# Optimization experiments

Hardware: AMD Instinct MI355X
Metric: run time of the kernel (lower is better)

## Reference

```python
import jax, jax.numpy as jnp
import numpy as np

# Quantization constants (match init_kwargs)
A_SCALE = 0.05   # activation scale
W_SCALE = 0.01   # weight scale
A_QN, A_QP = -128, 127  # int8 activation clamp range
STRIDE = (2, 2)
PADDING = ((1, 1), (1, 1))
DILATION = (1, 1)


def setup_inputs() -> dict:
    key = jax.random.key(0)
    kx, kw = jax.random.split(key)
    # Input activations [N, C_in, H, W]
    x = jax.random.normal(kx, (32, 256, 56, 56), dtype=jnp.float32)
    # Int4 weights in [-8, 7], stored as int-valued float32 (unpacked form of weight_packed)
    w = jax.random.randint(kw, (256, 256, 3, 3), -8, 8).astype(jnp.float32)
    return {"x": x, "w": w}


def reference(x, w):
    # Activation int8 quantization: round-half-to-even (matches torch.round), clamp to [a_qn, a_qp]
    x_q = jnp.clip(jnp.round(x / A_SCALE), A_QN, A_QP)
    # Int4xInt8 GEMM over unfolded patches == conv on quantized integer values.
    # Values are small ints so fp32 accumulation is exact (|acc| <= 2304*127*8 < 2^24).
    acc = jax.lax.conv_general_dilated(
        x_q, w,
        window_strides=STRIDE,
        padding=PADDING,
        rhs_dilation=DILATION,
        dimension_numbers=("NCHW", "OIHW", "NCHW"),
    )  # [N, C_out, H_out, W_out] = [32, 256, 28, 28]
    # Dequantize: acc_int32 * (a_scale * w_scale); bias=False; out_dtype=float32
    y = acc * (A_SCALE * W_SCALE)
    return y.astype(jnp.float32)
```

## Files before the change

kernel.cpp:

```cpp
#include <hip/hip_runtime.h>
#include <stdint.h>

typedef int v4i __attribute__((ext_vector_type(4)));

#define N_IMG 32
#define C_IN 256
#define H_IN 56
#define W_IN 56
#define C_OUT 256
#define H_OUT 28
#define W_OUT 28
#define H_PAD 58
#define W_PAD 58
#define SP_TOT (N_IMG*H_OUT*W_OUT)

#define XPAD_BYTES ((size_t)N_IMG*H_PAD*W_PAD*C_IN)


__device__ __forceinline__ void glds16(const int8_t* g, int8_t* l) {
    __builtin_amdgcn_global_load_lds(
        (const __attribute__((address_space(1))) void*)g,
        (__attribute__((address_space(3))) void*)l, 16, 0, 0);
}

__global__ __launch_bounds__(256, 4) void quant_kernel(const float* __restrict__ x,
                                                       int8_t* __restrict__ xpad) {
    __shared__ uint32_t ldsu[W_IN * 65];
    const int hp = blockIdx.x, n = blockIdx.y;
    const int t = threadIdx.x;
    int8_t* row = xpad + ((size_t)n * H_PAD + hp) * W_PAD * C_IN;

    if (hp == 0 || hp == H_PAD - 1) {
        #pragma unroll
        for (int i = 0; i < 4; ++i) {
            int idx = i * 256 + t;
            if (idx < 928) *(int4*)(row + idx * 16) = (int4){0, 0, 0, 0};
        }
        return;
    }
    const int h = hp - 1;
    const float* xrow = x + (size_t)n * (C_IN * H_IN * W_IN) + (size_t)h * W_IN;

    if (t < 32) {
        int8_t* p = (t < 16) ? (row + t * 16)
                             : (row + (size_t)(W_PAD - 1) * C_IN + (t - 16) * 16);
        *(int4*)p = (int4){0, 0, 0, 0};
    }

    const int lane = t & 63, wv = t >> 6;
    const int j = lane >> 4, w4 = lane & 15;
    const int w4c = (w4 < 14) ? w4 : 13;
    #pragma unroll
    for (int i16 = 0; i16 < 16; ++i16) {
        const int c4p = i16 * 4 + wv;
        const float4 v = *(const float4*)(xrow + (size_t)(4 * c4p + j) * (H_IN * W_IN)
                                          + w4c * 4);
        float f[4] = {v.x, v.y, v.z, v.w};
        uint32_t u = 0;
        #pragma unroll
        for (int i = 0; i < 4; ++i) {
            float qv = rintf(f[i] * 20.0f);
            qv = fminf(fmaxf(qv, -128.0f), 127.0f);
            u |= ((uint32_t)((int)qv & 255)) << (8 * i);
        }
        uint32_t p1 = __shfl_xor(u, 16);
        uint32_t tt = (j & 1) ? (((p1 >> 8) & 0x00FF00FFu) | (u & 0xFF00FF00u))
                              : ((u & 0x00FF00FFu) | ((p1 << 8) & 0xFF00FF00u));
        uint32_t p2 = __shfl_xor(tt, 32);
        uint32_t rr = (j & 2) ? ((p2 >> 16) | (tt & 0xFFFF0000u))
                              : ((tt & 0x0000FFFFu) | (p2 << 16));
        if (w4 < 14) ldsu[(w4 * 4 + j) * 65 + c4p] = rr;
    }
    __syncthreads();

    int8_t* op = row + C_IN;
    #pragma unroll
    for (int it = 0; it < 14; ++it) {
        int idx = it * 256 + t;
        int w = idx >> 6, c4 = idx & 63;
        *(uint32_t*)(op + (size_t)w * C_IN + c4 * 4) = ldsu[w * 65 + c4];
    }
}

__global__ __launch_bounds__(256) void wq_kernel(const float* __restrict__ w,
                                                 int8_t* __restrict__ wq) {
    int idx = blockIdx.x * 256 + threadIdx.x;
    int ci  = idx & 255;
    int co  = (idx >> 8) & 255;
    int khw = idx >> 16;
    float v = w[(size_t)(co * C_IN + ci) * 9 + khw];
    wq[idx] = (int8_t)(int)rintf(v);
}

__global__ __launch_bounds__(256, 4) void conv_kernel(const int8_t* __restrict__ xpad,
                                                      const int8_t* __restrict__ wq,
                                                      float* __restrict__ out) {
    __shared__ __align__(16) int8_t lds[36864];
    const int t = threadIdx.x;
    const int wave = t >> 6, lane = t & 63;
    const int q = lane >> 4, s = lane & 15;

    const int wg = blockIdx.x;
    const int lg = (wg & 7) * 98 + (wg >> 3);
    const int co_blk = (lg & 1) * 128;
    const int sp_blk = (lg >> 1) * 64;

    const int srow = t >> 2;
    const int scl  = t & 3;
    const int sq   = scl ^ ((srow >> 1) & 3);
    const int8_t* gw0 = wq + (size_t)(co_blk + srow) * 256 + sq * 16;
    const int8_t* gw1 = wq + (size_t)(co_blk + 64 + srow) * 256 + sq * 16;
    const int spA = sp_blk + srow;
    const int nA  = spA / (H_OUT * W_OUT);
    const int rmA = spA - nA * (H_OUT * W_OUT);
    const int hoA = rmA / W_OUT;
    const int woA = rmA - hoA * W_OUT;
    const int8_t* ga = xpad + ((size_t)(nA * H_PAD + hoA * 2) * W_PAD + woA * 2) * C_IN
                       + sq * 16;

    const int cw = (wave >> 1) * 64;
    const int sw = (wave & 1) * 32;
    int out_base[2];
    #pragma unroll
    for (int jj = 0; jj < 2; ++jj) {
        int sp = sp_blk + sw + jj * 16 + s;
        int n  = sp / (H_OUT * W_OUT);
        int rm = sp - n * (H_OUT * W_OUT);
        int ho = rm / W_OUT;
        int wo = rm - ho * W_OUT;
        out_base[jj] = n * (C_OUT * H_OUT * W_OUT) + ho * W_OUT + wo;
    }

    v4i acc[4][2];
    #pragma unroll
    for (int i = 0; i < 4; ++i)
        #pragma unroll
        for (int jj = 0; jj < 2; ++jj)
            acc[i][jj] = (v4i){0, 0, 0, 0};

    auto stage = [&](int hk, int8_t* lb) {
        const int tap = hk >> 2, sl = hk & 3;
        const int wo_ = tap * (C_OUT * C_IN) + sl * 64;
        const int ao_ = ((tap / 3) * W_PAD + (tap % 3)) * C_IN + sl * 64;
        glds16(gw0 + wo_, lb + t * 16);
        glds16(gw1 + wo_, lb + 4096 + t * 16);
        glds16(ga  + ao_, lb + 8192 + t * 16);
    };

    auto compute = [&](const int8_t* lb) {
        const int stoff = (q ^ ((s >> 1) & 3)) * 16;
        v4i a[4], b[2];
        #pragma unroll
        for (int i = 0; i < 4; ++i)
            a[i] = *(const v4i*)(lb + (cw + i * 16 + s) * 64 + stoff);
        #pragma unroll
        for (int jj = 0; jj < 2; ++jj)
            b[jj] = *(const v4i*)(lb + 8192 + (sw + jj * 16 + s) * 64 + stoff);
        #pragma unroll
        for (int i = 0; i < 4; ++i)
            #pragma unroll
            for (int jj = 0; jj < 2; ++jj)
                acc[i][jj] = __builtin_amdgcn_mfma_i32_16x16x64_i8(
                    a[i], b[jj], acc[i][jj], 0, 0, 0);
    };

    stage(0, lds);
    stage(1, lds + 12288);
    #pragma unroll
    for (int hk = 0; hk < 36; ++hk) {
        if (hk < 35)
            asm volatile("s_waitcnt vmcnt(3)\n\ts_barrier" ::: "memory");
        else
            asm volatile("s_waitcnt vmcnt(0)\n\ts_barrier" ::: "memory");
        if (hk + 2 < 36) stage(hk + 2, lds + ((hk + 2) % 3) * 12288);
        compute(lds + (hk % 3) * 12288);
    }

    #pragma unroll
    for (int jj = 0; jj < 2; ++jj) {
        #pragma unroll
        for (int i = 0; i < 4; ++i) {
            const int co0 = co_blk + cw + i * 16 + q * 4;
            #pragma unroll
            for (int r = 0; r < 4; ++r) {
                out[(size_t)out_base[jj] + (size_t)(co0 + r) * (H_OUT * W_OUT)] =
                    (float)acc[i][jj][r] * 0.0005f;
            }
        }
    }
}

extern "C" void kernel_launch(void* const* d_in, const int* in_sizes, int n_in,
                              void* d_out, int out_size, void* d_ws, size_t ws_size,
                              hipStream_t stream) {
    const float* x = (const float*)d_in[0];
    const float* w = (const float*)d_in[1];
    float* out = (float*)d_out;
    int8_t* xpad = (int8_t*)d_ws;
    int8_t* wqb  = xpad + XPAD_BYTES;

    quant_kernel<<<dim3(H_PAD, N_IMG), 256, 0, stream>>>(x, xpad);
    wq_kernel<<<(9 * C_OUT * C_IN) / 256, 256, 0, stream>>>(w, wqb);
    conv_kernel<<<dim3(784), 256, 0, stream>>>(xpad, wqb, out);
}
```

Measured before the change: 196.7 us.

## Enlarge conv tile to 128x128 and fold weight quantization into quant kernel

The conv workgroup tile doubles along the spatial dimension from 128x64 to 128x128. Each wave now computes a 64x64 output block with 16 accumulators, which gives more MFMA work per LDS load and halves the number of workgroups to 392. Weight quantization now runs in extra blocks of the activation quant kernel, which removes one kernel launch. In exchange, each block needs more LDS and registers (launch bounds drop to 3 waves per SIMD), and 392 workgroups may underfill the 256 CUs.

```diff
diff --git a/kernel.cpp b/kernel.cpp
--- a/kernel.cpp
+++ b/kernel.cpp
@@ -24,10 +24,29 @@
 }
 
 __global__ __launch_bounds__(256, 4) void quant_kernel(const float* __restrict__ x,
-                                                       int8_t* __restrict__ xpad) {
+                                                       int8_t* __restrict__ xpad,
+                                                       const float* __restrict__ w,
+                                                       int8_t* __restrict__ wq) {
     __shared__ uint32_t ldsu[W_IN * 65];
     const int hp = blockIdx.x, n = blockIdx.y;
     const int t = threadIdx.x;
+
+    if (n >= N_IMG) {
+        const int base = ((n - N_IMG) * H_PAD + hp) * 1024;
+        #pragma unroll
+        for (int i = 0; i < 4; ++i) {
+            int idx = base + i * 256 + t;
+            if (idx < 9 * C_OUT * C_IN) {
+                int ci  = idx & 255;
+                int co  = (idx >> 8) & 255;
+                int khw = idx >> 16;
+                float v = w[(size_t)(co * C_IN + ci) * 9 + khw];
+                wq[idx] = (int8_t)(int)rintf(v);
+            }
+        }
+        return;
+    }
+
     int8_t* row = xpad + ((size_t)n * H_PAD + hp) * W_PAD * C_IN;
 
     if (hp == 0 || hp == H_PAD - 1) {
@@ -77,52 +96,51 @@
     #pragma unroll
     for (int it = 0; it < 14; ++it) {
         int idx = it * 256 + t;
-        int w = idx >> 6, c4 = idx & 63;
-        *(uint32_t*)(op + (size_t)w * C_IN + c4 * 4) = ldsu[w * 65 + c4];
-    }
-}
-
-__global__ __launch_bounds__(256) void wq_kernel(const float* __restrict__ w,
-                                                 int8_t* __restrict__ wq) {
-    int idx = blockIdx.x * 256 + threadIdx.x;
-    int ci  = idx & 255;
-    int co  = (idx >> 8) & 255;
-    int khw = idx >> 16;
-    float v = w[(size_t)(co * C_IN + ci) * 9 + khw];
-    wq[idx] = (int8_t)(int)rintf(v);
-}
-
-__global__ __launch_bounds__(256, 4) void conv_kernel(const int8_t* __restrict__ xpad,
+        int w_ = idx >> 6, c4 = idx & 63;
+        *(uint32_t*)(op + (size_t)w_ * C_IN + c4 * 4) = ldsu[w_ * 65 + c4];
+    }
+}
+
+__global__ __launch_bounds__(256, 3) void conv_kernel(const int8_t* __restrict__ xpad,
                                                       const int8_t* __restrict__ wq,
                                                       float* __restrict__ out) {
-    __shared__ __align__(16) int8_t lds[36864];
+    __shared__ __align__(16) int8_t lds[49152];
     const int t = threadIdx.x;
     const int wave = t >> 6, lane = t & 63;
     const int q = lane >> 4, s = lane & 15;
 
     const int wg = blockIdx.x;
-    const int lg = (wg & 7) * 98 + (wg >> 3);
+    const int lg = (wg & 7) * 49 + (wg >> 3);
     const int co_blk = (lg & 1) * 128;
-    const int sp_blk = (lg >> 1) * 64;
+    const int sp_blk = (lg >> 1) * 128;
 
     const int srow = t >> 2;
     const int scl  = t & 3;
     const int sq   = scl ^ ((srow >> 1) & 3);
     const int8_t* gw0 = wq + (size_t)(co_blk + srow) * 256 + sq * 16;
     const int8_t* gw1 = wq + (size_t)(co_blk + 64 + srow) * 256 + sq * 16;
-    const int spA = sp_blk + srow;
-    const int nA  = spA / (H_OUT * W_OUT);
-    const int rmA = spA - nA * (H_OUT * W_OUT);
-    const int hoA = rmA / W_OUT;
-    const int woA = rmA - hoA * W_OUT;
-    const int8_t* ga = xpad + ((size_t)(nA * H_PAD + hoA * 2) * W_PAD + woA * 2) * C_IN
-                       + sq * 16;
+    const int8_t* ga0;
+    const int8_t* ga1;
+    {
+        int spA = sp_blk + srow;
+        int nA  = spA / (H_OUT * W_OUT);
+        int rmA = spA - nA * (H_OUT * W_OUT);
+        int hoA = rmA / W_OUT;
+        int woA = rmA - hoA * W_OUT;
+        ga0 = xpad + ((size_t)(nA * H_PAD + hoA * 2) * W_PAD + woA * 2) * C_IN + sq * 16;
+        int spB = sp_blk + 64 + srow;
+        int nB  = spB / (H_OUT * W_OUT);
+        int rmB = spB - nB * (H_OUT * W_OUT);
+        int hoB = rmB / W_OUT;
+        int woB = rmB - hoB * W_OUT;
+        ga1 = xpad + ((size_t)(nB * H_PAD + hoB * 2) * W_PAD + woB * 2) * C_IN + sq * 16;
+    }
 
     const int cw = (wave >> 1) * 64;
-    const int sw = (wave & 1) * 32;
-    int out_base[2];
-    #pragma unroll
-    for (int jj = 0; jj < 2; ++jj) {
+    const int sw = (wave & 1) * 64;
+    int out_base[4];
+    #pragma unroll
+    for (int jj = 0; jj < 4; ++jj) {
         int sp = sp_blk + sw + jj * 16 + s;
         int n  = sp / (H_OUT * W_OUT);
         int rm = sp - n * (H_OUT * W_OUT);
@@ -131,11 +149,11 @@
         out_base[jj] = n * (C_OUT * H_OUT * W_OUT) + ho * W_OUT + wo;
     }
 
-    v4i acc[4][2];
+    v4i acc[4][4];
     #pragma unroll
     for (int i = 0; i < 4; ++i)
         #pragma unroll
-        for (int jj = 0; jj < 2; ++jj)
+        for (int jj = 0; jj < 4; ++jj)
             acc[i][jj] = (v4i){0, 0, 0, 0};
 
     auto stage = [&](int hk, int8_t* lb) {
@@ -144,40 +162,41 @@
         const int ao_ = ((tap / 3) * W_PAD + (tap % 3)) * C_IN + sl * 64;
         glds16(gw0 + wo_, lb + t * 16);
         glds16(gw1 + wo_, lb + 4096 + t * 16);
-        glds16(ga  + ao_, lb + 8192 + t * 16);
+        glds16(ga0 + ao_, lb + 8192 + t * 16);
+        glds16(ga1 + ao_, lb + 12288 + t * 16);
     };
 
     auto compute = [&](const int8_t* lb) {
         const int stoff = (q ^ ((s >> 1) & 3)) * 16;
-        v4i a[4], b[2];
+        v4i a[4], b[4];
         #pragma unroll
         for (int i = 0; i < 4; ++i)
             a[i] = *(const v4i*)(lb + (cw + i * 16 + s) * 64 + stoff);
         #pragma unroll
-        for (int jj = 0; jj < 2; ++jj)
+        for (int jj = 0; jj < 4; ++jj)
             b[jj] = *(const v4i*)(lb + 8192 + (sw + jj * 16 + s) * 64 + stoff);
         #pragma unroll
         for (int i = 0; i < 4; ++i)
             #pragma unroll
-            for (int jj = 0; jj < 2; ++jj)
+            for (int jj = 0; jj < 4; ++jj)
                 acc[i][jj] = __builtin_amdgcn_mfma_i32_16x16x64_i8(
                     a[i], b[jj], acc[i][jj], 0, 0, 0);
     };
 
     stage(0, lds);
-    stage(1, lds + 12288);
+    stage(1, lds + 16384);
     #pragma unroll
     for (int hk = 0; hk < 36; ++hk) {
         if (hk < 35)
-            asm volatile("s_waitcnt vmcnt(3)\n\ts_barrier" ::: "memory");
+            asm volatile("s_waitcnt vmcnt(4)\n\ts_barrier" ::: "memory");
         else
             asm volatile("s_waitcnt vmcnt(0)\n\ts_barrier" ::: "memory");
-        if (hk + 2 < 36) stage(hk + 2, lds + ((hk + 2) % 3) * 12288);
-        compute(lds + (hk % 3) * 12288);
-    }
-
-    #pragma unroll
-    for (int jj = 0; jj < 2; ++jj) {
+        if (hk + 2 < 36) stage(hk + 2, lds + ((hk + 2) % 3) * 16384);
+        compute(lds + (hk % 3) * 16384);
+    }
+
+    #pragma unroll
+    for (int jj = 0; jj < 4; ++jj) {
         #pragma unroll
         for (int i = 0; i < 4; ++i) {
             const int co0 = co_blk + cw + i * 16 + q * 4;
@@ -199,7 +218,6 @@
     int8_t* xpad = (int8_t*)d_ws;
     int8_t* wqb  = xpad + XPAD_BYTES;
 
-    quant_kernel<<<dim3(H_PAD, N_IMG), 256, 0, stream>>>(x, xpad);
-    wq_kernel<<<(9 * C_OUT * C_IN) / 256, 256, 0, stream>>>(w, wqb);
-    conv_kernel<<<dim3(784), 256, 0, stream>>>(xpad, wqb, out);
-}
+    quant_kernel<<<dim3(H_PAD, N_IMG + 10), 256, 0, stream>>>(x, xpad, w, wqb);
+    conv_kernel<<<dim3(392), 256, 0, stream>>>(xpad, wqb, out);
+}
```

Measured after the change: 184.7 us (median of 2 runs). 1.07x faster.
